# Kernel tuning notes

Measured on AMD Instinct MI355X. Metric: run time of the kernel, lower is better.

The kernel has to match this reference:

```python
import jax, jax.numpy as jnp
import numpy as np
import math

B, S, H, D = 1, 2048, 12, 128
DIM = H * D
BLKQ, BLKK = 128, 64
TOPK = 0.2
EPS = 1e-6
NEG = -1e30


def setup_inputs() -> dict:
    key = jax.random.key(0)
    ks = jax.random.split(key, 8)
    hidden_states = jax.random.normal(ks[0], (B, S, DIM), jnp.float32)
    # interleaved RoPE tables: even slots hold cos, odd slots hold sin phase copies
    pos = np.arange(S, dtype=np.float64)[:, None]
    inv = 1.0 / (10000.0 ** (np.arange(0, D, 2, dtype=np.float64) / D))
    ang = pos * inv[None, :]                       # [S, D/2]
    freqs_cos = jnp.asarray(np.repeat(np.cos(ang), 2, axis=-1), jnp.float32).reshape(1, S, 1, D)
    freqs_sin = jnp.asarray(np.repeat(np.sin(ang), 2, axis=-1), jnp.float32).reshape(1, S, 1, D)
    sc = 1.0 / math.sqrt(DIM)
    Wq = jax.random.normal(ks[1], (DIM, DIM), jnp.float32) * sc
    Wk = jax.random.normal(ks[2], (DIM, DIM), jnp.float32) * sc
    Wv = jax.random.normal(ks[3], (DIM, DIM), jnp.float32) * sc
    Wo = jax.random.normal(ks[4], (DIM, DIM), jnp.float32) * sc
    bq = jax.random.normal(ks[5], (DIM,), jnp.float32) * 0.01
    bk = jax.random.normal(ks[6], (DIM,), jnp.float32) * 0.01
    bv = jax.random.normal(ks[7], (DIM,), jnp.float32) * 0.01
    bo = jnp.zeros((DIM,), jnp.float32)
    gq = jnp.ones((DIM,), jnp.float32)
    gk = jnp.ones((DIM,), jnp.float32)
    return dict(hidden_states=hidden_states, freqs_cos=freqs_cos, freqs_sin=freqs_sin,
                Wq=Wq, bq=bq, Wk=Wk, bk=bk, Wv=Wv, bv=bv, Wo=Wo, bo=bo, gq=gq, gk=gk)


def _rmsnorm(x, g):
    return x * jax.lax.rsqrt(jnp.mean(x * x, axis=-1, keepdims=True) + EPS) * g


def _rope(x, fc, fs):
    # x: [B,S,H,D]; interleaved even/odd rotation as in _apply_rotary_emb
    x1 = x[..., 0::2]
    x2 = x[..., 1::2]
    cos = fc[..., 0::2]
    sin = fs[..., 1::2]
    even = x1 * cos - x2 * sin
    odd = x1 * sin + x2 * cos
    return jnp.stack([even, odd], axis=-1).reshape(x.shape)


def _sla(q, k, v):
    # q,k,v: [B,H,S,D]. Top-k block-sparse exact attention + linear attention
    # (softmax feature map) on the unselected blocks, jointly normalized.
    nqb, nkb = S // BLKQ, S // BLKK
    ksel = max(1, int(math.ceil(TOPK * nkb)))
    qb = q.reshape(B, H, nqb, BLKQ, D).mean(axis=3)
    kb = k.reshape(B, H, nkb, BLKK, D).mean(axis=3)
    blk_scores = jnp.einsum('bhqd,bhkd->bhqk', qb, kb)
    _, idx = jax.lax.top_k(blk_scores, ksel)                  # [B,H,nqb,ksel]
    bmask = (jax.nn.one_hot(idx, nkb, dtype=jnp.float32).sum(axis=-2) > 0)
    mask = jnp.repeat(jnp.repeat(bmask, BLKQ, axis=2), BLKK, axis=3)  # [B,H,S,S]

    scale = 1.0 / math.sqrt(D)
    s = jnp.einsum('bhqd,bhkd->bhqk', q, k) * scale
    m = jnp.max(jnp.where(mask, s, NEG), axis=-1, keepdims=True)
    p = jnp.where(mask, jnp.exp(s - m), 0.0)
    num_s = jnp.einsum('bhqk,bhkd->bhqd', p, v)
    den_s = p.sum(axis=-1, keepdims=True)

    lq = jax.nn.softmax(q, axis=-1)
    lk = jax.nn.softmax(k, axis=-1)
    L = jnp.where(mask, 0.0, jnp.einsum('bhqd,bhkd->bhqk', lq, lk))
    num_l = jnp.einsum('bhqk,bhkd->bhqd', L, v)
    den_l = L.sum(axis=-1, keepdims=True)

    w = jnp.exp(-m)  # bring linear part onto the max-shifted exp scale
    return (num_s + w * num_l) / (den_s + w * den_l)


def reference(hidden_states, freqs_cos, freqs_sin, Wq, bq, Wk, bk, Wv, bv, Wo, bo, gq, gk):
    q = _rmsnorm(hidden_states @ Wq + bq, gq).reshape(B, S, H, D)
    k = _rmsnorm(hidden_states @ Wk + bk, gk).reshape(B, S, H, D)
    v = (hidden_states @ Wv + bv).reshape(B, S, H, D)
    q = _rope(q, freqs_cos, freqs_sin)
    k = _rope(k, freqs_cos, freqs_sin)
    q, k, v = (t.transpose(0, 2, 1, 3) for t in (q, k, v))  # [B,H,S,D]
    o = _sla(q, k, v)
    o = o.transpose(0, 2, 1, 3).reshape(B, S, DIM)
    return o @ Wo + bo
```

## Files before the change

### kernel.cpp

```cpp
#include <hip/hip_runtime.h>
#include <hip/hip_bf16.h>

#define SQ   2048
#define DIMM 1536
#define QS   4608
#define NH   12
#define DH   128
#define NQB  16
#define NKB  32
#define KSEL 7

typedef unsigned short u16;
typedef __bf16 bf16x8 __attribute__((ext_vector_type(8)));
typedef _Float16 f16x8 __attribute__((ext_vector_type(8)));
typedef short  s16x8  __attribute__((ext_vector_type(8)));
typedef float  f32x4  __attribute__((ext_vector_type(4)));
typedef u16    u16x4  __attribute__((ext_vector_type(4)));

__device__ __forceinline__ float bf2f(u16 u) {
  unsigned int x = ((unsigned int)u) << 16;
  return __builtin_bit_cast(float, x);
}
__device__ __forceinline__ u16 f2bf(float f) {
  unsigned int x = __builtin_bit_cast(unsigned int, f);
  x += 0x7fffu + ((x >> 16) & 1u);
  return (u16)(x >> 16);
}

typedef __attribute__((address_space(3))) void lds_vt;
typedef const __attribute__((address_space(1))) void g_vt;
__device__ __forceinline__ void dma16(const void* g, void* l) {
  __builtin_amdgcn_global_load_lds((g_vt*)g, (lds_vt*)l, 16, 0, 0);
}

__global__ __launch_bounds__(256) void prep_all(const float* __restrict__ hs,
                                                u16* __restrict__ hh,
                                                u16* __restrict__ hl,
                                                const float* __restrict__ W0,
                                                const float* __restrict__ W1,
                                                const float* __restrict__ W2,
                                                const float* __restrict__ W3,
                                                u16* __restrict__ WTh,
                                                u16* __restrict__ WTl) {
  __shared__ float tile[64][65];
  int bx = blockIdx.x;
  if (bx < 1536) {
    size_t i = ((size_t)bx * 256 + threadIdx.x) * 8;
    f32x4 a = *(const f32x4*)&hs[i];
    f32x4 b = *(const f32x4*)&hs[i + 4];
    s16x8 h, l;
    #pragma unroll
    for (int j = 0; j < 4; j++) {
      u16 hj = f2bf(a[j]); h[j] = (short)hj; l[j] = (short)f2bf(a[j] - bf2f(hj));
      u16 hk = f2bf(b[j]); h[4 + j] = (short)hk; l[4 + j] = (short)f2bf(b[j] - bf2f(hk));
    }
    *(s16x8*)&hh[i] = h;
    *(s16x8*)&hl[i] = l;
    return;
  }
  int b2 = bx - 1536;
  int wi = b2 / 576;
  int rest = b2 % 576;
  int k0 = (rest / 24) * 64, n0 = (rest % 24) * 64;
  const float* W = (wi == 0) ? W0 : (wi == 1) ? W1 : (wi == 2) ? W2 : W3;
  int x = threadIdx.x & 63, y = threadIdx.x >> 6;
  #pragma unroll
  for (int i = 0; i < 16; i++) {
    int k = y + i * 4;
    tile[k][x] = W[(size_t)(k0 + k) * DIMM + n0 + x];
  }
  __syncthreads();
  size_t obase = (size_t)wi * DIMM * DIMM;
  #pragma unroll
  for (int rep = 0; rep < 2; rep++) {
    int u = threadIdx.x + rep * 256;
    int n = u >> 3, c8 = u & 7;
    s16x8 hv, lv;
    #pragma unroll
    for (int e = 0; e < 8; e++) {
      float v = tile[c8 * 8 + e][n];
      if (wi == 3) {
        hv[e] = (short)__builtin_bit_cast(u16, (_Float16)v);
      } else {
        u16 hb = f2bf(v);
        hv[e] = (short)hb;
        lv[e] = (short)f2bf(v - bf2f(hb));
      }
    }
    size_t oi = obase + (size_t)(n0 + n) * DIMM + k0 + c8 * 8;
    *(s16x8*)&WTh[oi] = hv;
    if (wi != 3) *(s16x8*)&WTl[oi] = lv;
  }
}

__global__ __launch_bounds__(512, 4) void gemm3_k(const u16* __restrict__ Ahp,
                                                  const u16* __restrict__ Alp,
                                                  const u16* __restrict__ WTh,
                                                  const u16* __restrict__ WTl,
                                                  const float* __restrict__ bq,
                                                  const float* __restrict__ bk,
                                                  const float* __restrict__ bv,
                                                  float* __restrict__ C,
                                                  u16* __restrict__ vbfT) {
  __shared__ u16 As[2][128][64];
  __shared__ u16 Bs[2][128][64];
  const int tid = threadIdx.x;
  const int w = tid >> 6, lane = tid & 63, quad = lane >> 4, l16 = lane & 15;
  const int wr = w >> 2, wc = w & 3;
  const int m_base = blockIdx.y * 128;
  const int nt = blockIdx.x;
  const int wi = nt / 12;
  const int n_in = (nt % 12) * 128;
  const u16* Bh0 = WTh + ((size_t)wi * DIMM + n_in) * DIMM;
  const u16* Bl0 = WTl + ((size_t)wi * DIMM + n_in) * DIMM;
  const float* bias = (wi == 0) ? bq : (wi == 1) ? bk : bv;
  const bool split = (wi != 2);

  const int srow = lane >> 3;
  const int skc = (((lane & 7) ^ srow) * 8);
  const int rx = (l16 & 7);

  f32x4 zero4 = {0.f, 0.f, 0.f, 0.f};
  f32x4 acc[4][2];
  #pragma unroll
  for (int i = 0; i < 4; i++)
    #pragma unroll
    for (int j = 0; j < 2; j++) acc[i][j] = zero4;

  for (int k0 = 0; k0 < DIMM; k0 += 64) {
    #pragma unroll
    for (int c = 0; c < 2; c++) {
      int r0 = w * 16 + c * 8;
      int row = r0 + srow;
      dma16(&Ahp[(size_t)(m_base + row) * DIMM + k0 + skc], &As[0][r0][0]);
      dma16(&Bh0[(size_t)row * DIMM + k0 + skc], &Bs[0][r0][0]);
      if (split) {
        dma16(&Alp[(size_t)(m_base + row) * DIMM + k0 + skc], &As[1][r0][0]);
        dma16(&Bl0[(size_t)row * DIMM + k0 + skc], &Bs[1][r0][0]);
      }
    }
    __syncthreads();
    #pragma unroll
    for (int kk = 0; kk < 2; kk++) {
      const int coff = ((kk * 4 + quad) ^ rx) * 8;
      bf16x8 afh[4], afl[4], bfh[2], bfl[2];
      #pragma unroll
      for (int i = 0; i < 4; i++)
        afh[i] = __builtin_bit_cast(bf16x8,
                 *(const s16x8*)&As[0][wr * 64 + i * 16 + l16][coff]);
      #pragma unroll
      for (int j = 0; j < 2; j++)
        bfh[j] = __builtin_bit_cast(bf16x8,
                 *(const s16x8*)&Bs[0][wc * 32 + j * 16 + l16][coff]);
      if (split) {
        #pragma unroll
        for (int i = 0; i < 4; i++)
          afl[i] = __builtin_bit_cast(bf16x8,
                   *(const s16x8*)&As[1][wr * 64 + i * 16 + l16][coff]);
        #pragma unroll
        for (int j = 0; j < 2; j++)
          bfl[j] = __builtin_bit_cast(bf16x8,
                   *(const s16x8*)&Bs[1][wc * 32 + j * 16 + l16][coff]);
      }
      #pragma unroll
      for (int i = 0; i < 4; i++)
        #pragma unroll
        for (int j = 0; j < 2; j++) {
          acc[i][j] = __builtin_amdgcn_mfma_f32_16x16x32_bf16(afh[i], bfh[j], acc[i][j], 0, 0, 0);
          if (split) {
            acc[i][j] = __builtin_amdgcn_mfma_f32_16x16x32_bf16(afh[i], bfl[j], acc[i][j], 0, 0, 0);
            acc[i][j] = __builtin_amdgcn_mfma_f32_16x16x32_bf16(afl[i], bfh[j], acc[i][j], 0, 0, 0);
          }
        }
    }
    __syncthreads();
  }

  if (wi != 2) {
    #pragma unroll
    for (int i = 0; i < 4; i++)
      #pragma unroll
      for (int j = 0; j < 2; j++) {
        int tc = wc * 32 + j * 16 + l16;
        float bv2 = bias[n_in + tc];
        #pragma unroll
        for (int rg = 0; rg < 4; rg++) {
          int r = m_base + wr * 64 + i * 16 + quad * 4 + rg;
          C[(size_t)r * QS + nt * 128 + tc] = acc[i][j][rg] + bv2;
        }
      }
  } else {
    int hh = nt % 12;
    int bblk = blockIdx.y * 2 + wr;
    u16* vb = vbfT + (size_t)(hh * NKB + bblk) * 8192;
    int kb8 = quad >> 1;
    int klo = (quad & 1) * 4;
    #pragma unroll
    for (int i = 0; i < 4; i++) {
      int k8 = (i * 2 + kb8);
      #pragma unroll
      for (int j = 0; j < 2; j++) {
        int d = wc * 32 + j * 16 + l16;
        float bv2 = bias[n_in + d];
        u16x4 o;
        #pragma unroll
        for (int rg = 0; rg < 4; rg++) o[rg] = f2bf(acc[i][j][rg] + bv2);
        *(u16x4*)&vb[d * 64 + ((k8 ^ (d & 7)) << 3) + klo] = o;
      }
    }
  }
}

__global__ __launch_bounds__(256) void gemm_o(const u16* __restrict__ Ap,
                                              const u16* __restrict__ Bp,
                                              const float* __restrict__ bias,
                                              float* __restrict__ C) {
  __shared__ u16 As[64][64];
  __shared__ u16 Bs[128][64];
  const int tid = threadIdx.x;
  const int w = tid >> 6, lane = tid & 63, quad = lane >> 4, l16 = lane & 15;
  const int wr = w >> 1, wc = w & 1;
  const int m_base = blockIdx.y * 64, n_base = blockIdx.x * 128;
  const int srow = lane >> 3;
  const int skc = (((lane & 7) ^ srow) * 8);
  const int rx = (l16 & 7);

  f32x4 zero4 = {0.f, 0.f, 0.f, 0.f};
  f32x4 acc[2][4];
  #pragma unroll
  for (int i = 0; i < 2; i++)
    #pragma unroll
    for (int j = 0; j < 4; j++) acc[i][j] = zero4;

  for (int k0 = 0; k0 < DIMM; k0 += 64) {
    #pragma unroll
    for (int c = 0; c < 2; c++) {
      int r0 = w * 16 + c * 8;
      int row = r0 + srow;
      dma16(&Ap[(size_t)(m_base + row) * DIMM + k0 + skc], &As[r0][0]);
    }
    #pragma unroll
    for (int c = 0; c < 4; c++) {
      int r0 = w * 32 + c * 8;
      int row = r0 + srow;
      dma16(&Bp[(size_t)(n_base + row) * DIMM + k0 + skc], &Bs[r0][0]);
    }
    __syncthreads();
    #pragma unroll
    for (int kk = 0; kk < 2; kk++) {
      const int coff = ((kk * 4 + quad) ^ rx) * 8;
      f16x8 af[2], bf[4];
      #pragma unroll
      for (int i = 0; i < 2; i++)
        af[i] = __builtin_bit_cast(f16x8,
                *(const s16x8*)&As[wr * 32 + i * 16 + l16][coff]);
      #pragma unroll
      for (int j = 0; j < 4; j++)
        bf[j] = __builtin_bit_cast(f16x8,
                *(const s16x8*)&Bs[wc * 64 + j * 16 + l16][coff]);
      #pragma unroll
      for (int i = 0; i < 2; i++)
        #pragma unroll
        for (int j = 0; j < 4; j++)
          acc[i][j] = __builtin_amdgcn_mfma_f32_16x16x32_f16(af[i], bf[j], acc[i][j], 0, 0, 0);
    }
    __syncthreads();
  }
  #pragma unroll
  for (int i = 0; i < 2; i++)
    #pragma unroll
    for (int j = 0; j < 4; j++) {
      int c = n_base + wc * 64 + j * 16 + l16;
      float bv2 = bias[c];
      #pragma unroll
      for (int rg = 0; rg < 4; rg++) {
        int r = m_base + wr * 32 + i * 16 + quad * 4 + rg;
        C[(size_t)r * DIMM + c] = acc[i][j][rg] + bv2;
      }
    }
}

__global__ __launch_bounds__(256) void norm_rope_k(float* __restrict__ qkv,
                                                   const float* __restrict__ gq,
                                                   const float* __restrict__ gk,
                                                   const float* __restrict__ fc,
                                                   const float* __restrict__ fs,
                                                   u16* __restrict__ qbf,
                                                   u16* __restrict__ kbf) {
  int s = blockIdx.x;
  float* row = qkv + (size_t)s * QS + (blockIdx.y == 0 ? 0 : DIMM);
  const float* g = (blockIdx.y == 0) ? gq : gk;
  u16* obase = (blockIdx.y == 0) ? qbf : kbf;
  int t = threadIdx.x;
  float ss = 0.f;
  #pragma unroll
  for (int i = 0; i < 6; i++) {
    float v = row[t + i * 256];
    ss += v * v;
  }
  #pragma unroll
  for (int m = 1; m < 64; m <<= 1) ss += __shfl_xor(ss, m, 64);
  __shared__ float wsum[4];
  if ((t & 63) == 0) wsum[t >> 6] = ss;
  __syncthreads();
  float tot = wsum[0] + wsum[1] + wsum[2] + wsum[3];
  float sc = rsqrtf(tot / 1536.0f + 1e-6f);
  #pragma unroll
  for (int i = 0; i < 3; i++) {
    int p = t + i * 256;
    int h = p >> 6, ip = p & 63;
    int base = h * 128 + 2 * ip;
    float x1 = row[base] * sc * g[base];
    float x2 = row[base + 1] * sc * g[base + 1];
    float c = fc[(size_t)s * 128 + 2 * ip];
    float sn = fs[(size_t)s * 128 + 2 * ip + 1];
    float ev = x1 * c - x2 * sn;
    float od = x1 * sn + x2 * c;
    row[base]     = ev;
    row[base + 1] = od;
    int gsk = ip >> 2, e = (2 * ip) & 7;
    int cc = (gsk & 8) | ((gsk ^ (s & 7)) & 7);
    u16* ob = obase + ((size_t)h * SQ + s) * 128;
    unsigned int pack = (unsigned int)f2bf(ev) | ((unsigned int)f2bf(od) << 16);
    *(unsigned int*)&ob[cc * 8 + e] = pack;
  }
}

__global__ __launch_bounds__(256) void kvmeans_k(const float* __restrict__ qf,
                                                 const float* __restrict__ kf,
                                                 const u16* __restrict__ vbfT,
                                                 float* __restrict__ KV,
                                                 float* __restrict__ slk,
                                                 float* __restrict__ qb,
                                                 float* __restrict__ kb) {
  __shared__ u16 lkT[128 * 72];
  __shared__ u16 vtT[128 * 64];
  int h = blockIdx.y, t = threadIdx.x;
  if (blockIdx.x >= NKB) {
    int mx = blockIdx.x - NKB;
    if (t < 128) {
      if (mx < NQB) {
        float a = 0.f;
        for (int r = 0; r < 128; r++) a += qf[(size_t)(mx * 128 + r) * QS + h * DH + t];
        qb[(h * NQB + mx) * DH + t] = a * (1.0f / 128.0f);
      } else {
        int ki = mx - NQB;
        float a = 0.f;
        for (int r = 0; r < 64; r++) a += kf[(size_t)(ki * 64 + r) * QS + h * DH + t];
        kb[(h * NKB + ki) * DH + t] = a * (1.0f / 64.0f);
      }
    }
    return;
  }
  int kbi = blockIdx.x;
  int w = t >> 6, lane = t & 63, quad = lane >> 4, l16 = lane & 15;

  {
    const u16* vsrc = vbfT + ((size_t)(h * NKB + kbi)) * 128 * 64;
    #pragma unroll
    for (int c = 0; c < 4; c++)
      dma16(vsrc + (w * 32 + c * 8) * 64 + lane * 8, &vtT[(w * 32 + c * 8) * 64]);
  }
  {
    int r = t >> 2, q4 = t & 3;
    const float* kr = kf + (size_t)(kbi * 64 + r) * QS + h * DH;
    f32x4 x[8];
    float mx = -3.4e38f;
    #pragma unroll
    for (int i = 0; i < 8; i++) {
      x[i] = *(const f32x4*)&kr[q4 * 32 + i * 4];
      mx = fmaxf(mx, fmaxf(fmaxf(x[i][0], x[i][1]), fmaxf(x[i][2], x[i][3])));
    }
    mx = fmaxf(mx, __shfl_xor(mx, 1, 64));
    mx = fmaxf(mx, __shfl_xor(mx, 2, 64));
    float sum = 0.f;
    #pragma unroll
    for (int i = 0; i < 8; i++)
      #pragma unroll
      for (int e = 0; e < 4; e++) { float v = __expf(x[i][e] - mx); x[i][e] = v; sum += v; }
    sum += __shfl_xor(sum, 1, 64);
    sum += __shfl_xor(sum, 2, 64);
    float inv = 1.0f / sum;
    #pragma unroll
    for (int i = 0; i < 8; i++)
      #pragma unroll
      for (int e = 0; e < 4; e++)
        lkT[(q4 * 32 + i * 4 + e) * 72 + r] = f2bf(x[i][e] * inv);
  }
  __syncthreads();

  f32x4 zero4 = {0.f, 0.f, 0.f, 0.f};
  f32x4 acc[2][8];
  #pragma unroll
  for (int i = 0; i < 2; i++)
    #pragma unroll
    for (int j = 0; j < 8; j++) acc[i][j] = zero4;
  #pragma unroll
  for (int kk = 0; kk < 2; kk++) {
    bf16x8 af[2];
    #pragma unroll
    for (int i = 0; i < 2; i++)
      af[i] = __builtin_bit_cast(bf16x8,
              *(const s16x8*)&lkT[(w * 32 + i * 16 + l16) * 72 + kk * 32 + quad * 8]);
    const int voff = ((kk * 4 + quad) ^ (l16 & 7)) * 8;
    #pragma unroll
    for (int j = 0; j < 8; j++) {
      bf16x8 vb = __builtin_bit_cast(bf16x8, *(const s16x8*)&vtT[(j * 16 + l16) * 64 + voff]);
      #pragma unroll
      for (int i = 0; i < 2; i++)
        acc[i][j] = __builtin_amdgcn_mfma_f32_16x16x32_bf16(af[i], vb, acc[i][j], 0, 0, 0);
    }
  }
  float* out = KV + (size_t)(h * NKB + kbi) * 16384;
  #pragma unroll
  for (int i = 0; i < 2; i++)
    #pragma unroll
    for (int j = 0; j < 8; j++) {
      #pragma unroll
      for (int rg = 0; rg < 4; rg++) {
        int r = w * 32 + i * 16 + quad * 4 + rg;
        int c = j * 16 + l16;
        out[(size_t)r * 128 + c] = acc[i][j][rg];
      }
    }
  if (t < 128) {
    float a = 0.f;
    #pragma unroll
    for (int c8 = 0; c8 < 8; c8++) {
      s16x8 v8 = *(const s16x8*)&lkT[t * 72 + c8 * 8];
      #pragma unroll
      for (int e = 0; e < 8; e++) a += bf2f((u16)v8[e]);
    }
    slk[(h * NKB + kbi) * DH + t] = a;
  }
}

__global__ __launch_bounds__(256) void kvtot_topk_k(const float* __restrict__ KV,
                                                    const float* __restrict__ slk,
                                                    const float* __restrict__ qb,
                                                    const float* __restrict__ kb,
                                                    float* __restrict__ KVtot,
                                                    float* __restrict__ sltot,
                                                    int* __restrict__ sel) {
  int h = blockIdx.y, t = threadIdx.x;
  if (blockIdx.x < 64) {
    int e = blockIdx.x * 256 + t;
    float a = 0.f;
    for (int b = 0; b < NKB; b++) a += KV[(size_t)(h * NKB + b) * 16384 + e];
    KVtot[(size_t)h * 16384 + e] = a;
    if (blockIdx.x == 0 && t < 128) {
      float s2 = 0.f;
      for (int b = 0; b < NKB; b++) s2 += slk[(h * NKB + b) * DH + t];
      sltot[h * DH + t] = s2;
    }
    return;
  }
  int qi = blockIdx.x - 64;
  __shared__ float scs[NKB];
  int r = t >> 3, sub = t & 7;
  const float* qv = qb + (size_t)(h * NQB + qi) * DH;
  const float* kv2 = kb + (size_t)(h * NKB + r) * DH;
  float a = 0.f;
  #pragma unroll
  for (int dd = 0; dd < 16; dd++) a += qv[sub * 16 + dd] * kv2[sub * 16 + dd];
  a += __shfl_xor(a, 1, 64);
  a += __shfl_xor(a, 2, 64);
  a += __shfl_xor(a, 4, 64);
  if (sub == 0) scs[r] = a;
  __syncthreads();
  if (t == 0) {
    unsigned int used = 0;
    for (int it = 0; it < KSEL; it++) {
      float best = -3.4e38f; int bi = 0;
      for (int j = 0; j < NKB; j++)
        if (!((used >> j) & 1) && scs[j] > best) { best = scs[j]; bi = j; }
      used |= 1u << bi;
      sel[(h * NQB + qi) * 8 + it] = bi;
    }
  }
}

__global__ __launch_bounds__(256) void mt_k(const int* __restrict__ sel,
                                            const float* __restrict__ KV,
                                            const float* __restrict__ KVtot,
                                            u16* __restrict__ MTg) {
  __shared__ u16 MT[128 * 136];
  __shared__ int selsh[KSEL];
  int h = blockIdx.y, q2 = blockIdx.x, tid = threadIdx.x;
  if (tid < KSEL) selsh[tid] = sel[(h * NQB + q2) * 8 + tid];
  __syncthreads();
  for (int i = 0; i < 16; i++) {
    int idx = i * 256 + tid;
    int e4 = idx * 4;
    int d1 = e4 >> 7, d2 = e4 & 127;
    f32x4 a = *(const f32x4*)&KVtot[(size_t)h * 16384 + e4];
    #pragma unroll
    for (int k2 = 0; k2 < KSEL; k2++) {
      f32x4 s4 = *(const f32x4*)&KV[(size_t)(h * NKB + selsh[k2]) * 16384 + e4];
      a -= s4;
    }
    #pragma unroll
    for (int j = 0; j < 4; j++) MT[(d2 + j) * 136 + d1] = f2bf(a[j]);
  }
  __syncthreads();
  u16* out = MTg + (size_t)(h * NQB + q2) * 16384;
  #pragma unroll
  for (int i = 0; i < 8; i++) {
    int u = i * 256 + tid;
    int r = u >> 4, kc = u & 15;
    int sc = (kc & 8) | ((kc ^ (r & 7)) & 7);
    *(s16x8*)&out[r * 128 + sc * 8] = *(const s16x8*)&MT[r * 136 + kc * 8];
  }
}

__global__ __launch_bounds__(256) void attn_k(const u16* __restrict__ qbf,
                                              const u16* __restrict__ kbf,
                                              const u16* __restrict__ vbfT,
                                              const int* __restrict__ sel,
                                              const float* __restrict__ slk,
                                              const float* __restrict__ sltot,
                                              const u16* __restrict__ MTg,
                                              u16* __restrict__ of16) {
  __shared__ u16 smem[29184];
  __shared__ float mrow[64], lrow[64], dent[64], slsh[128];
  __shared__ int selsh[KSEL];
  u16* qt  = smem;
  u16* kt  = smem + 8192;
  u16* vtT = smem + 16384;
  u16* ptb = smem + 24576;
  u16* MT  = smem + 8192;

  int h = blockIdx.y, qi = blockIdx.x, tid = threadIdx.x;
  int w = tid >> 6, lane = tid & 63, quad = lane >> 4, l16 = lane & 15;

  {
    const u16* qsrc = qbf + ((size_t)h * SQ + qi * 64) * 128;
    #pragma unroll
    for (int c = 0; c < 4; c++)
      dma16(qsrc + (w * 16 + c * 4) * 128 + lane * 8, &qt[(w * 16 + c * 4) * 128]);
  }
  if (tid < KSEL) selsh[tid] = sel[(h * NQB + (qi >> 1)) * 8 + tid];
  __syncthreads();

  float m_run[4], l_run[4];
  f32x4 zero4 = {0.f, 0.f, 0.f, 0.f};
  f32x4 oacc[8];
  #pragma unroll
  for (int rg = 0; rg < 4; rg++) { m_run[rg] = -3.0e38f; l_run[rg] = 0.f; }
  #pragma unroll
  for (int nt = 0; nt < 8; nt++) oacc[nt] = zero4;

  for (int bi = 0; bi < KSEL; bi++) {
    int b = selsh[bi];
    {
      const u16* ksrc = kbf + ((size_t)h * SQ + b * 64) * 128;
      #pragma unroll
      for (int c = 0; c < 4; c++)
        dma16(ksrc + (w * 16 + c * 4) * 128 + lane * 8, &kt[(w * 16 + c * 4) * 128]);
      const u16* vsrc = vbfT + ((size_t)(h * NKB + b)) * 128 * 64;
      #pragma unroll
      for (int c = 0; c < 4; c++)
        dma16(vsrc + (w * 32 + c * 8) * 64 + lane * 8, &vtT[(w * 32 + c * 8) * 64]);
    }
    __syncthreads();

    f32x4 sacc[4];
    #pragma unroll
    for (int nt = 0; nt < 4; nt++) sacc[nt] = zero4;
    __builtin_amdgcn_s_setprio(1);
    #pragma unroll
    for (int kk = 0; kk < 4; kk++) {
      const int kkq = kk * 4 + quad;
      const int qoff = ((kkq & 8) | ((kkq ^ (l16 & 7)) & 7)) * 8;
      bf16x8 af = __builtin_bit_cast(bf16x8, *(const s16x8*)&qt[(w * 16 + l16) * 128 + qoff]);
      #pragma unroll
      for (int nt = 0; nt < 4; nt++) {
        bf16x8 bfr = __builtin_bit_cast(bf16x8, *(const s16x8*)&kt[(nt * 16 + l16) * 128 + qoff]);
        sacc[nt] = __builtin_amdgcn_mfma_f32_16x16x32_bf16(af, bfr, sacc[nt], 0, 0, 0);
      }
    }
    __builtin_amdgcn_s_setprio(0);
    const float SCALE = 0.08838834764831845f;
    #pragma unroll
    for (int nt = 0; nt < 4; nt++) sacc[nt] *= SCALE;

    #pragma unroll
    for (int rg = 0; rg < 4; rg++) {
      float bmax = fmaxf(fmaxf(sacc[0][rg], sacc[1][rg]),
                         fmaxf(sacc[2][rg], sacc[3][rg]));
      bmax = fmaxf(bmax, __shfl_xor(bmax, 1, 64));
      bmax = fmaxf(bmax, __shfl_xor(bmax, 2, 64));
      bmax = fmaxf(bmax, __shfl_xor(bmax, 4, 64));
      bmax = fmaxf(bmax, __shfl_xor(bmax, 8, 64));
      float mold = m_run[rg];
      float mnew = fmaxf(mold, bmax);
      float alpha = __expf(mold - mnew);
      float rs = 0.f;
      #pragma unroll
      for (int nt = 0; nt < 4; nt++) {
        float p = __expf(sacc[nt][rg] - mnew);
        sacc[nt][rg] = p; rs += p;
      }
      rs += __shfl_xor(rs, 1, 64);
      rs += __shfl_xor(rs, 2, 64);
      rs += __shfl_xor(rs, 4, 64);
      rs += __shfl_xor(rs, 8, 64);
      m_run[rg] = mnew;
      l_run[rg] = l_run[rg] * alpha + rs;
      #pragma unroll
      for (int nt = 0; nt < 8; nt++) oacc[nt][rg] *= alpha;
    }
    #pragma unroll
    for (int rg = 0; rg < 4; rg++) {
      int r = w * 16 + quad * 4 + rg;
      #pragma unroll
      for (int nt = 0; nt < 4; nt++) ptb[r * 72 + nt * 16 + l16] = f2bf(sacc[nt][rg]);
    }

    __builtin_amdgcn_s_setprio(1);
    #pragma unroll
    for (int kk = 0; kk < 2; kk++) {
      bf16x8 pa = __builtin_bit_cast(bf16x8, *(const s16x8*)&ptb[(w * 16 + l16) * 72 + kk * 32 + quad * 8]);
      #pragma unroll
      for (int nt = 0; nt < 8; nt++) {
        const int voff = ((kk * 4 + quad) ^ (l16 & 7)) * 8;
        bf16x8 vb = __builtin_bit_cast(bf16x8, *(const s16x8*)&vtT[(nt * 16 + l16) * 64 + voff]);
        oacc[nt] = __builtin_amdgcn_mfma_f32_16x16x32_bf16(pa, vb, oacc[nt], 0, 0, 0);
      }
    }
    __builtin_amdgcn_s_setprio(0);
    __syncthreads();
  }

  {
    const u16* mtb = MTg + (size_t)(h * NQB + (qi >> 1)) * 16384;
    #pragma unroll
    for (int c = 0; c < 8; c++)
      dma16(mtb + (w * 32 + c * 4) * 128 + lane * 8, &MT[(w * 32 + c * 4) * 128]);
  }
  if (l16 == 0) {
    #pragma unroll
    for (int rg = 0; rg < 4; rg++) {
      int r = w * 16 + quad * 4 + rg;
      mrow[r] = m_run[rg];
      lrow[r] = l_run[rg];
    }
  }
  if (tid < 128) {
    float a = sltot[h * DH + tid];
    #pragma unroll
    for (int i = 0; i < KSEL; i++) a -= slk[(h * NKB + selsh[i]) * DH + tid];
    slsh[tid] = a;
  }
  __syncthreads();

  {
    int r = tid >> 2, sub = tid & 3;
    float w_r = __expf(-mrow[r]);
    float mx = -3.4e38f;
    #pragma unroll
    for (int gi = 0; gi < 4; gi++) {
      int gc = sub * 4 + gi;
      int c = (gc & 8) | ((gc ^ (r & 7)) & 7);
      #pragma unroll
      for (int e = 0; e < 8; e++) mx = fmaxf(mx, bf2f(qt[r * 128 + c * 8 + e]));
    }
    mx = fmaxf(mx, __shfl_xor(mx, 1, 64));
    mx = fmaxf(mx, __shfl_xor(mx, 2, 64));
    float sum = 0.f;
    #pragma unroll
    for (int gi = 0; gi < 4; gi++) {
      int gc = sub * 4 + gi;
      int c = (gc & 8) | ((gc ^ (r & 7)) & 7);
      #pragma unroll
      for (int e = 0; e < 8; e++) sum += __expf(bf2f(qt[r * 128 + c * 8 + e]) - mx);
    }
    sum += __shfl_xor(sum, 1, 64);
    sum += __shfl_xor(sum, 2, 64);
    float sc2 = w_r / sum;
    float dl = 0.f;
    #pragma unroll
    for (int gi = 0; gi < 4; gi++) {
      int gc = sub * 4 + gi;
      int c = (gc & 8) | ((gc ^ (r & 7)) & 7);
      #pragma unroll
      for (int e = 0; e < 8; e++) {
        float lq = __expf(bf2f(qt[r * 128 + c * 8 + e]) - mx) * sc2;
        dl += lq * slsh[gc * 8 + e];
        qt[r * 128 + c * 8 + e] = f2bf(lq);
      }
    }
    dl += __shfl_xor(dl, 1, 64);
    dl += __shfl_xor(dl, 2, 64);
    if (sub == 0) dent[r] = lrow[r] + dl;
  }
  __syncthreads();

  __builtin_amdgcn_s_setprio(1);
  #pragma unroll
  for (int kk = 0; kk < 4; kk++) {
    const int kkq = kk * 4 + quad;
    const int qoff = ((kkq & 8) | ((kkq ^ (l16 & 7)) & 7)) * 8;
    bf16x8 af = __builtin_bit_cast(bf16x8, *(const s16x8*)&qt[(w * 16 + l16) * 128 + qoff]);
    #pragma unroll
    for (int nt = 0; nt < 8; nt++) {
      const int kc = kk * 4 + quad;
      const int mo = ((kc & 8) | ((kc ^ (l16 & 7)) & 7)) * 8;
      bf16x8 mb = __builtin_bit_cast(bf16x8, *(const s16x8*)&MT[(nt * 16 + l16) * 128 + mo]);
      oacc[nt] = __builtin_amdgcn_mfma_f32_16x16x32_bf16(af, mb, oacc[nt], 0, 0, 0);
    }
  }
  __builtin_amdgcn_s_setprio(0);

  #pragma unroll
  for (int rg = 0; rg < 4; rg++) {
    int r = w * 16 + quad * 4 + rg;
    float inv = 1.0f / dent[r];
    #pragma unroll
    for (int nt = 0; nt < 8; nt++) {
      int c = nt * 16 + l16;
      float v = oacc[nt][rg] * inv;
      size_t oi = (size_t)(qi * 64 + r) * DIMM + h * DH + c;
      of16[oi] = __builtin_bit_cast(u16, (_Float16)v);
    }
  }
}

extern "C" void kernel_launch(void* const* d_in, const int* in_sizes, int n_in,
                              void* d_out, int out_size, void* d_ws, size_t ws_size,
                              hipStream_t stream) {
  const float* hs = (const float*)d_in[0];
  const float* fc = (const float*)d_in[1];
  const float* fs = (const float*)d_in[2];
  const float* Wq = (const float*)d_in[3];
  const float* bq = (const float*)d_in[4];
  const float* Wk = (const float*)d_in[5];
  const float* bk = (const float*)d_in[6];
  const float* Wv = (const float*)d_in[7];
  const float* bv = (const float*)d_in[8];
  const float* Wo = (const float*)d_in[9];
  const float* bo = (const float*)d_in[10];
  const float* gq = (const float*)d_in[11];
  const float* gk = (const float*)d_in[12];

  char* p = (char*)d_ws;
  auto alloc = [&](size_t bytes) {
    char* r = p; p += (bytes + 255) & ~(size_t)255; return r;
  };
  u16* WTh = (u16*)alloc((size_t)4 * DIMM * DIMM * 2);
  u16* WTl = (u16*)alloc((size_t)4 * DIMM * DIMM * 2);
  u16* hsh = (u16*)alloc((size_t)SQ * DIMM * 2);
  u16* hsl = (u16*)alloc((size_t)SQ * DIMM * 2);
  float* qkv = (float*)alloc((size_t)SQ * QS * 4);
  u16* qbf = (u16*)alloc((size_t)NH * SQ * DH * 2);
  u16* kbf = (u16*)alloc((size_t)NH * SQ * DH * 2);
  u16* vbfT = (u16*)alloc((size_t)NH * NKB * DH * 64 * 2);
  float* qb = (float*)alloc((size_t)NH * NQB * DH * 4);
  float* kb = (float*)alloc((size_t)NH * NKB * DH * 4);
  int* sel = (int*)alloc((size_t)NH * NQB * 8 * 4);
  float* KV = (float*)alloc((size_t)NH * NKB * DH * DH * 4);
  float* slk = (float*)alloc((size_t)NH * NKB * DH * 4);
  float* KVtot = (float*)alloc((size_t)NH * DH * DH * 4);
  float* sltot = (float*)alloc((size_t)NH * DH * 4);

  float* qf = qkv;
  float* kf = qkv + DIMM;

  prep_all<<<1536 + 2304, 256, 0, stream>>>(hs, hsh, hsl, Wq, Wk, Wv, Wo, WTh, WTl);

  gemm3_k<<<dim3(36, 16), 512, 0, stream>>>(hsh, hsl, WTh, WTl, bq, bk, bv, qkv, vbfT);

  norm_rope_k<<<dim3(SQ, 2), 256, 0, stream>>>(qkv, gq, gk, fc, fs, qbf, kbf);
  kvmeans_k<<<dim3(NKB + NQB + NKB, NH), 256, 0, stream>>>(qf, kf, vbfT, KV, slk, qb, kb);
  kvtot_topk_k<<<dim3(64 + NQB, NH), 256, 0, stream>>>(KV, slk, qb, kb, KVtot, sltot, sel);

  u16* of16 = hsh;
  u16* MTg = hsl;
  mt_k<<<dim3(NQB, NH), 256, 0, stream>>>(sel, KV, KVtot, MTg);
  attn_k<<<dim3(2 * NQB, NH), 256, 0, stream>>>(qbf, kbf, vbfT, sel, slk, sltot, MTg, of16);

  const u16* WTo = WTh + (size_t)3 * DIMM * DIMM;
  gemm_o<<<dim3(12, 32), 256, 0, stream>>>(of16, WTo, bo, (float*)d_out);
}
```

Measured before the change: 308.3 us.

## Swizzle GEMM block order, shrink attention LDS, cache softmax inputs in registers

Both GEMMs now launch as 1D grids and remap block IDs so consecutive blocks spread across the 8 XCDs, grouping tiles that share operands to improve L2 reuse. The attention kernel aliases the P buffer onto the K tile region to cut shared memory, which may allow higher occupancy. Two extra barriers are added per KV iteration to make that aliasing safe. The linear-attention softmax over q now keeps the 32 per-thread values in registers instead of re-reading LDS and recomputing exp, at the cost of more register pressure.

Measured after the change: 326.3 us. 1.06x slower.

```diff
diff --git a/kernel.cpp b/kernel.cpp
--- a/kernel.cpp
+++ b/kernel.cpp
@@ -107,8 +107,11 @@
   const int tid = threadIdx.x;
   const int w = tid >> 6, lane = tid & 63, quad = lane >> 4, l16 = lane & 15;
   const int wr = w >> 2, wc = w & 3;
-  const int m_base = blockIdx.y * 128;
-  const int nt = blockIdx.x;
+  const int bid = blockIdx.x;
+  const int swz = (bid & 7) * 72 + (bid >> 3);
+  const int nt = swz >> 4;
+  const int mi = swz & 15;
+  const int m_base = mi * 128;
   const int wi = nt / 12;
   const int n_in = (nt % 12) * 128;
   const u16* Bh0 = WTh + ((size_t)wi * DIMM + n_in) * DIMM;
@@ -191,7 +194,7 @@
       }
   } else {
     int hh = nt % 12;
-    int bblk = blockIdx.y * 2 + wr;
+    int bblk = mi * 2 + wr;
     u16* vb = vbfT + (size_t)(hh * NKB + bblk) * 8192;
     int kb8 = quad >> 1;
     int klo = (quad & 1) * 4;
@@ -220,7 +223,9 @@
   const int tid = threadIdx.x;
   const int w = tid >> 6, lane = tid & 63, quad = lane >> 4, l16 = lane & 15;
   const int wr = w >> 1, wc = w & 1;
-  const int m_base = blockIdx.y * 64, n_base = blockIdx.x * 128;
+  const int bid = blockIdx.x;
+  const int swz = (bid & 7) * 48 + (bid >> 3);
+  const int m_base = (swz & 31) * 64, n_base = (swz >> 5) * 128;
   const int srow = lane >> 3;
   const int skc = (((lane & 7) ^ srow) * 8);
   const int rx = (l16 & 7);
@@ -521,13 +526,13 @@
                                               const float* __restrict__ sltot,
                                               const u16* __restrict__ MTg,
                                               u16* __restrict__ of16) {
-  __shared__ u16 smem[29184];
+  __shared__ u16 smem[25600];
   __shared__ float mrow[64], lrow[64], dent[64], slsh[128];
   __shared__ int selsh[KSEL];
   u16* qt  = smem;
-  u16* kt  = smem + 8192;
-  u16* vtT = smem + 16384;
-  u16* ptb = smem + 24576;
+  u16* vtT = smem + 8192;
+  u16* kt  = smem + 16384;
+  u16* ptb = smem + 16384;
   u16* MT  = smem + 8192;
 
   int h = blockIdx.y, qi = blockIdx.x, tid = threadIdx.x;
@@ -610,12 +615,14 @@
       #pragma unroll
       for (int nt = 0; nt < 8; nt++) oacc[nt][rg] *= alpha;
     }
+    __syncthreads();
     #pragma unroll
     for (int rg = 0; rg < 4; rg++) {
       int r = w * 16 + quad * 4 + rg;
       #pragma unroll
       for (int nt = 0; nt < 4; nt++) ptb[r * 72 + nt * 16 + l16] = f2bf(sacc[nt][rg]);
     }
+    __syncthreads();
 
     __builtin_amdgcn_s_setprio(1);
     #pragma unroll
@@ -657,24 +664,30 @@
   {
     int r = tid >> 2, sub = tid & 3;
     float w_r = __expf(-mrow[r]);
+    float xr[32];
     float mx = -3.4e38f;
     #pragma unroll
     for (int gi = 0; gi < 4; gi++) {
       int gc = sub * 4 + gi;
       int c = (gc & 8) | ((gc ^ (r & 7)) & 7);
       #pragma unroll
-      for (int e = 0; e < 8; e++) mx = fmaxf(mx, bf2f(qt[r * 128 + c * 8 + e]));
+      for (int e = 0; e < 8; e++) {
+        float v = bf2f(qt[r * 128 + c * 8 + e]);
+        xr[gi * 8 + e] = v;
+        mx = fmaxf(mx, v);
+      }
     }
     mx = fmaxf(mx, __shfl_xor(mx, 1, 64));
     mx = fmaxf(mx, __shfl_xor(mx, 2, 64));
     float sum = 0.f;
     #pragma unroll
-    for (int gi = 0; gi < 4; gi++) {
-      int gc = sub * 4 + gi;
-      int c = (gc & 8) | ((gc ^ (r & 7)) & 7);
-      #pragma unroll
-      for (int e = 0; e < 8; e++) sum += __expf(bf2f(qt[r * 128 + c * 8 + e]) - mx);
-    }
+    for (int gi = 0; gi < 4; gi++)
+      #pragma unroll
+      for (int e = 0; e < 8; e++) {
+        float v = __expf(xr[gi * 8 + e] - mx);
+        xr[gi * 8 + e] = v;
+        sum += v;
+      }
     sum += __shfl_xor(sum, 1, 64);
     sum += __shfl_xor(sum, 2, 64);
     float sc2 = w_r / sum;
@@ -685,7 +698,7 @@
       int c = (gc & 8) | ((gc ^ (r & 7)) & 7);
       #pragma unroll
       for (int e = 0; e < 8; e++) {
-        float lq = __expf(bf2f(qt[r * 128 + c * 8 + e]) - mx) * sc2;
+        float lq = xr[gi * 8 + e] * sc2;
         dl += lq * slsh[gc * 8 + e];
         qt[r * 128 + c * 8 + e] = f2bf(lq);
       }
@@ -768,7 +781,7 @@
 
   prep_all<<<1536 + 2304, 256, 0, stream>>>(hs, hsh, hsl, Wq, Wk, Wv, Wo, WTh, WTl);
 
-  gemm3_k<<<dim3(36, 16), 512, 0, stream>>>(hsh, hsl, WTh, WTl, bq, bk, bv, qkv, vbfT);
+  gemm3_k<<<576, 512, 0, stream>>>(hsh, hsl, WTh, WTl, bq, bk, bv, qkv, vbfT);
 
   norm_rope_k<<<dim3(SQ, 2), 256, 0, stream>>>(qkv, gq, gk, fc, fs, qbf, kbf);
   kvmeans_k<<<dim3(NKB + NQB + NKB, NH), 256, 0, stream>>>(qf, kf, vbfT, KV, slk, qb, kb);
@@ -780,5 +793,5 @@
   attn_k<<<dim3(2 * NQB, NH), 256, 0, stream>>>(qbf, kbf, vbfT, sel, slk, sltot, MTg, of16);
 
   const u16* WTo = WTh + (size_t)3 * DIMM * DIMM;
-  gemm_o<<<dim3(12, 32), 256, 0, stream>>>(of16, WTo, bo, (float*)d_out);
-}
+  gemm_o<<<384, 256, 0, stream>>>(of16, WTo, bo, (float*)d_out);
+}
```
